# Performance work log

Measured on AMD Instinct MI355X. Metric: run time of the kernel, lower is better.

## Reference

```python
import jax, jax.numpy as jnp
import numpy as np

N = 100_000   # nodes
E = 600_000   # edges per layer (avg degree ~6, ogbn-arxiv-like)
IN, H, C = 128, 256, 40


def _sage_layer(x, src, dst, w_self, w_neigh, b):
    """DGL SAGEConv with mean aggregator: fc_self(x) + fc_neigh(mean_nbr) + b."""
    n = x.shape[0]
    msg = x[src]                                               # [E, d] gather
    agg = jax.ops.segment_sum(msg, dst, num_segments=n)        # [N, d]
    deg = jax.ops.segment_sum(jnp.ones((src.shape[0],), x.dtype), dst,
                              num_segments=n)                  # [N]
    h_neigh = agg / jnp.maximum(deg, 1.0)[:, None]             # mean; 0 if isolated
    return x @ w_self.T + h_neigh @ w_neigh.T + b


def setup_inputs() -> dict:
    key = jax.random.key(0)
    ks = jax.random.split(key, 11)
    s = 0.02
    return {
        "x": jax.random.normal(ks[0], (N, IN), jnp.float32),
        "src1": jax.random.randint(ks[1], (E,), 0, N, jnp.int32),
        "dst1": jax.random.randint(ks[2], (E,), 0, N, jnp.int32),
        "src2": jax.random.randint(ks[3], (E,), 0, N, jnp.int32),
        "dst2": jax.random.randint(ks[4], (E,), 0, N, jnp.int32),
        "w_self1": s * jax.random.normal(ks[5], (H, IN), jnp.float32),
        "w_neigh1": s * jax.random.normal(ks[6], (H, IN), jnp.float32),
        "b1": jnp.zeros((H,), jnp.float32),
        "w_self2": s * jax.random.normal(ks[7], (C, H), jnp.float32),
        "w_neigh2": s * jax.random.normal(ks[8], (C, H), jnp.float32),
        "b2": jnp.zeros((C,), jnp.float32),
    }


def reference(x, src1, dst1, src2, dst2, w_self1, w_neigh1, b1,
              w_self2, w_neigh2, b2):
    h = jax.nn.relu(_sage_layer(x, src1, dst1, w_self1, w_neigh1, b1))
    return _sage_layer(h, src2, dst2, w_self2, w_neigh2, b2)
```

## Files before the change

### kernel.cpp

```cpp
#include <hip/hip_runtime.h>
#include <hip/hip_bf16.h>
#include <cstdint>
#include <cstddef>


#define D_IN 128
#define D_H  256
#define D_C  40

#define NBLK     128
#define NBKT_MAX 392
#define BKT_CAP  2560

typedef __bf16 bf16_t;
typedef __attribute__((ext_vector_type(8))) __bf16 bf16x8;
typedef __attribute__((ext_vector_type(4))) __bf16 bf16x4;
typedef __attribute__((ext_vector_type(4))) float  f32x4;

static constexpr size_t NMAX = 100000;
static constexpr size_t EMAX = 600000;
static constexpr size_t NSC_MAX = (size_t)NBKT_MAX * NBLK;
static constexpr size_t alignup(size_t v) { return (v + 255) & ~size_t(255); }

static constexpr size_t HG1_OFF  = 0;
static constexpr size_t HG2_OFF  = alignup(HG1_OFF + NSC_MAX * 4);
static constexpr size_t BS1_OFF  = alignup(HG2_OFF + NSC_MAX * 4);
static constexpr size_t BS2_OFF  = alignup(BS1_OFF + 512 * 4);
static constexpr size_t RP1_OFF  = alignup(BS2_OFF + 512 * 4);
static constexpr size_t RP2_OFF  = alignup(RP1_OFF + (NMAX + 1) * 4);
static constexpr size_t BKT1_OFF = alignup(RP2_OFF + (NMAX + 1) * 4);
static constexpr size_t BKT2_OFF = alignup(BKT1_OFF + EMAX * 4);
static constexpr size_t XCAT_OFF = alignup(BKT2_OFF + EMAX * 4);
static constexpr size_t P_OFF    = alignup(XCAT_OFF + (NMAX + 64) * 256 * 2);
static constexpr size_t W1F_OFF  = alignup(P_OFF + NMAX * 40 * 2);
static constexpr size_t W2F_OFF  = alignup(W1F_OFF + 32 * 256 * 8 * 2);
static constexpr size_t WS_NEEDED = W2F_OFF + 32 * 80 * 8 * 2;

__global__ __launch_bounds__(256) void k_prep(
    const float* __restrict__ x, bf16_t* __restrict__ xcat,
    const float* __restrict__ ws1, const float* __restrict__ wn1,
    const float* __restrict__ ws2, const float* __restrict__ wn2,
    bf16_t* __restrict__ w1f, bf16_t* __restrict__ w2f,
    const int* __restrict__ dst1, const int* __restrict__ dst2,
    int* __restrict__ hg1, int* __restrict__ hg2,
    int N, int E, int chunk, int nbkt, int nconvx) {
  __shared__ int h[NBKT_MAX];
  int bid = blockIdx.x;

  if (bid < nconvx) {
    int t = bid * 256 + threadIdx.x;
    if (t < N * 16) {
      int row = t >> 4, j = t & 15;
      const float* sp = x + (size_t)row * 128 + j * 8;
      float4 v0 = ((const float4*)sp)[0];
      float4 v1 = ((const float4*)sp)[1];
      bf16x8 o;
      o[0] = (bf16_t)v0.x; o[1] = (bf16_t)v0.y; o[2] = (bf16_t)v0.z; o[3] = (bf16_t)v0.w;
      o[4] = (bf16_t)v1.x; o[5] = (bf16_t)v1.y; o[6] = (bf16_t)v1.z; o[7] = (bf16_t)v1.w;
      *(bf16x8*)(xcat + (size_t)row * 256 + j * 8) = o;
    }
    return;
  }
  bid -= nconvx;

  if (bid < 32) {
    int t = bid * 256 + threadIdx.x;
    {
      int ks4g = t >> 8, col = t & 255;
      int k0 = (ks4g >> 2) * 32 + (ks4g & 3) * 8;
      bf16x8 o;
#pragma unroll
      for (int i = 0; i < 8; ++i) {
        int k = k0 + i;
        float v = (k < 128) ? ws1[col * 128 + k] : wn1[col * 128 + (k - 128)];
        o[i] = (bf16_t)v;
      }
      *(bf16x8*)(w1f + (size_t)t * 8) = o;
    }
    if (t < 32 * 80) {
      int ks4g = t / 80, col = t - ks4g * 80;
      int k0 = (ks4g >> 2) * 32 + (ks4g & 3) * 8;
      bf16x8 o;
#pragma unroll
      for (int i = 0; i < 8; ++i) {
        int k = k0 + i;
        float v = (col < 40) ? ws2[col * 256 + k] : wn2[(col - 40) * 256 + k];
        o[i] = (bf16_t)v;
      }
      *(bf16x8*)(w2f + (size_t)t * 8) = o;
    }
    return;
  }
  bid -= 32;
  {
    const int* dst = (bid >> 7) ? dst2 : dst1;
    int*       hg  = (bid >> 7) ? hg2 : hg1;
    int        cb  = bid & 127;
    for (int i = threadIdx.x; i < nbkt; i += 256) h[i] = 0;
    __syncthreads();
    int beg = cb * chunk, end = min(E, beg + chunk);
    for (int e = beg + threadIdx.x; e < end; e += 256)
      atomicAdd(&h[dst[e] >> 8], 1);
    __syncthreads();
    for (int b = threadIdx.x; b < nbkt; b += 256)
      hg[b * NBLK + cb] = h[b];
  }
}

__global__ void k_scan_block(int* __restrict__ a1, int* __restrict__ a2,
                             int* __restrict__ b1s, int* __restrict__ b2s, int n) {
  int* a    = blockIdx.y ? a2 : a1;
  int* bsum = blockIdx.y ? b2s : b1s;
  __shared__ int lds[256];
  int t = threadIdx.x, i = blockIdx.x * 256 + t;
  int v = (i < n) ? a[i] : 0;
  lds[t] = v;
  __syncthreads();
  for (int off = 1; off < 256; off <<= 1) {
    int add = (t >= off) ? lds[t - off] : 0;
    __syncthreads();
    lds[t] += add;
    __syncthreads();
  }
  if (i < n) a[i] = lds[t] - v;
  if (t == 255) bsum[blockIdx.x] = lds[255];
}

__global__ void k_scat(const int* __restrict__ src1, const int* __restrict__ dst1,
                       const int* __restrict__ src2, const int* __restrict__ dst2,
                       const int* __restrict__ hg1, const int* __restrict__ hg2,
                       const int* __restrict__ b1s, const int* __restrict__ b2s,
                       unsigned* __restrict__ bkt1, unsigned* __restrict__ bkt2,
                       int E, int chunk, int nbkt, int nb) {
  const int* src = blockIdx.y ? src2 : src1;
  const int* dst = blockIdx.y ? dst2 : dst1;
  const int* hg  = blockIdx.y ? hg2 : hg1;
  const int* bs  = blockIdx.y ? b2s : b1s;
  unsigned*  bkt = blockIdx.y ? bkt2 : bkt1;
  const int cb = blockIdx.x, t = threadIdx.x;

  __shared__ int sbuf[256];
  __shared__ int sexcl[256];
  __shared__ int cur[NBKT_MAX];

  int v = (t < nb) ? bs[t] : 0;
  sbuf[t] = v;
  __syncthreads();
  for (int off = 1; off < 256; off <<= 1) {
    int add = (t >= off) ? sbuf[t - off] : 0;
    __syncthreads();
    sbuf[t] += add;
    __syncthreads();
  }
  sexcl[t] = sbuf[t] - v;
  __syncthreads();
  for (int i = t; i < nbkt; i += 256) {
    int idx = i * NBLK + cb;
    cur[i] = hg[idx] + sexcl[idx >> 8];
  }
  __syncthreads();

  int beg = cb * chunk, end = min(E, beg + chunk);
  for (int e = beg + t; e < end; e += 256) {
    int d = dst[e];
    int slot = atomicAdd(&cur[d >> 8], 1);
    bkt[slot] = (unsigned)src[e] | ((unsigned)(d & 255) << 24);
  }
}

__global__ __launch_bounds__(256) void k_bcsr(
    const int* __restrict__ hg1, const int* __restrict__ hg2,
    const int* __restrict__ b1s, const int* __restrict__ b2s,
    const unsigned* bkt1, const unsigned* bkt2,
    int* csr1, int* csr2,
    int* __restrict__ rp1, int* __restrict__ rp2, int E, int N, int nbkt, int nb) {
  const int* hg       = blockIdx.y ? hg2 : hg1;
  const int* bs       = blockIdx.y ? b2s : b1s;
  const unsigned* bkt = blockIdx.y ? bkt2 : bkt1;
  int* csr            = blockIdx.y ? csr2 : csr1;
  int* rowptr         = blockIdx.y ? rp2 : rp1;

  const int b = blockIdx.x, t = threadIdx.x;

  __shared__ int sbuf[256];
  __shared__ int hist[256];
  __shared__ int sc[256];
  __shared__ int cur[256];
  __shared__ int stage[BKT_CAP];
  __shared__ int s_base, s_endp;

  int v0 = (t < nb) ? bs[t] : 0;
  sbuf[t] = v0;
  __syncthreads();
  for (int off_ = 1; off_ < 256; off_ <<= 1) {
    int add = (t >= off_) ? sbuf[t - off_] : 0;
    __syncthreads();
    sbuf[t] += add;
    __syncthreads();
  }
  if (t == 0) {
    int i0 = b * NBLK;
    int e0 = sbuf[i0 >> 8] - ((i0 >> 8) < nb ? bs[i0 >> 8] : 0);
    s_base = hg[i0] + e0;
    if (b == nbkt - 1) {
      s_endp = E;
    } else {
      int i1 = (b + 1) * NBLK;
      int e1 = sbuf[i1 >> 8] - ((i1 >> 8) < nb ? bs[i1 >> 8] : 0);
      s_endp = hg[i1] + e1;
    }
  }
  hist[t] = 0;
  __syncthreads();
  const int base = s_base, endp = s_endp;
  const int cnt  = endp - base;

  for (int i = t; i < cnt; i += 256)
    atomicAdd(&hist[bkt[base + i] >> 24], 1);
  __syncthreads();

  int v = hist[t];
  sc[t] = v;
  __syncthreads();
  for (int off_ = 1; off_ < 256; off_ <<= 1) {
    int add = (t >= off_) ? sc[t - off_] : 0;
    __syncthreads();
    sc[t] += add;
    __syncthreads();
  }
  int excl = sc[t] - v;

  int node = b * 256 + t;
  if (node < N) rowptr[node] = base + excl;
  if (b == nbkt - 1 && t == 0) rowptr[N] = E;
  cur[t] = excl;
  __syncthreads();

  for (int i = t; i < cnt; i += 256) {
    unsigned u = bkt[base + i];
    int slot = atomicAdd(&cur[u >> 24], 1);
    if (slot < BKT_CAP) stage[slot] = (int)(u & 0xFFFFFFu);
  }
  __syncthreads();
  for (int i = t; i < cnt; i += 256)
    csr[base + i] = stage[i];
}

__global__ void k_agg1(bf16_t* __restrict__ xcat, const int* __restrict__ rowptr,
                       const int* __restrict__ csr, int N) {
  int t = blockIdx.x * 256 + threadIdx.x;
  int node = t >> 4, l = t & 15;
  if (node >= N) return;
  int beg = rowptr[node], end = rowptr[node + 1];
  float acc[8] = {0.f, 0.f, 0.f, 0.f, 0.f, 0.f, 0.f, 0.f};
  for (int e = beg; e < end; e += 4) {
    int e1 = e + 1 < end ? e + 1 : e;
    int e2 = e + 2 < end ? e + 2 : e;
    int e3 = e + 3 < end ? e + 3 : e;
    float m1 = e + 1 < end ? 1.f : 0.f;
    float m2 = e + 2 < end ? 1.f : 0.f;
    float m3 = e + 3 < end ? 1.f : 0.f;
    int s0 = csr[e], s1 = csr[e1], s2 = csr[e2], s3 = csr[e3];
    bf16x8 v0 = *(const bf16x8*)(xcat + (size_t)s0 * 256 + l * 8);
    bf16x8 v1 = *(const bf16x8*)(xcat + (size_t)s1 * 256 + l * 8);
    bf16x8 v2 = *(const bf16x8*)(xcat + (size_t)s2 * 256 + l * 8);
    bf16x8 v3 = *(const bf16x8*)(xcat + (size_t)s3 * 256 + l * 8);
#pragma unroll
    for (int i = 0; i < 8; ++i)
      acc[i] += (float)v0[i] + m1 * (float)v1[i] + m2 * (float)v2[i] + m3 * (float)v3[i];
  }
  float rd = (end > beg) ? 1.0f / (float)(end - beg) : 0.0f;
  bf16x8 o;
#pragma unroll
  for (int i = 0; i < 8; ++i) o[i] = (bf16_t)(acc[i] * rd);
  *(bf16x8*)(xcat + (size_t)node * 256 + 128 + l * 8) = o;
}

__global__ __launch_bounds__(256, 3) void k_fused(
    const bf16_t* __restrict__ xcat, const bf16_t* __restrict__ w1f,
    const float* __restrict__ b1, const bf16_t* __restrict__ w2f,
    const float* __restrict__ b2v, float* __restrict__ out,
    bf16_t* __restrict__ p, int N) {
  __shared__ __align__(16) char lds[32768];
  const int tid  = (int)threadIdx.x;
  const int wv   = tid >> 6;
  const int lane = tid & 63;
  const int lr   = lane & 15;
  const int lg   = lane >> 4;
  const int c0   = wv * 64;
  const int m0   = (int)blockIdx.x * 64;

  {
    const char* tb = (const char*)(xcat + (size_t)m0 * 256);
#pragma unroll
    for (int i = 0; i < 8; ++i) {
      int L   = i * 4096 + tid * 16;
      int row = L >> 9;
      int c   = L & 511;
      int so  = (row << 9) | (c ^ ((row & 7) << 4));
      __builtin_amdgcn_global_load_lds(
          (const __attribute__((address_space(1))) void*)(tb + so),
          (__attribute__((address_space(3))) void*)(lds + L), 16, 0, 0);
    }
  }

  bf16x8 wfc[4];
#pragma unroll
  for (int wb = 0; wb < 4; ++wb)
    wfc[wb] = *(const bf16x8*)(w1f + ((size_t)(0 * 4 + lg) * 256 +
                                      (c0 + wb * 16 + lr)) * 8);
  __syncthreads();

  bf16x8 axc[4];
#pragma unroll
  for (int rb = 0; rb < 4; ++rb) {
    int lrow = rb * 16 + lr;
    axc[rb] = *(const bf16x8*)(lds + lrow * 512 +
                               ((0 * 64 + lg * 16) ^ ((lrow & 7) << 4)));
  }

  f32x4 acc[4][4] = {};
#pragma unroll
  for (int ks = 0; ks < 8; ++ks) {
    bf16x8 wfn[4], axn[4];
    if (ks < 7) {
#pragma unroll
      for (int wb = 0; wb < 4; ++wb)
        wfn[wb] = *(const bf16x8*)(w1f + ((size_t)((ks + 1) * 4 + lg) * 256 +
                                          (c0 + wb * 16 + lr)) * 8);
#pragma unroll
      for (int rb = 0; rb < 4; ++rb) {
        int lrow = rb * 16 + lr;
        axn[rb] = *(const bf16x8*)(lds + lrow * 512 +
                                   (((ks + 1) * 64 + lg * 16) ^ ((lrow & 7) << 4)));
      }
    }
#pragma unroll
    for (int wb = 0; wb < 4; ++wb)
#pragma unroll
      for (int rb = 0; rb < 4; ++rb)
        acc[wb][rb] = __builtin_amdgcn_mfma_f32_16x16x32_bf16(
            wfc[wb], axc[rb], acc[wb][rb], 0, 0, 0);
    if (ks < 7) {
#pragma unroll
      for (int i = 0; i < 4; ++i) { wfc[i] = wfn[i]; axc[i] = axn[i]; }
    }
  }

  __syncthreads();

#pragma unroll
  for (int wb = 0; wb < 4; ++wb) {
    float4 b4 = *(const float4*)(b1 + c0 + wb * 16 + lg * 4);
#pragma unroll
    for (int rb = 0; rb < 4; ++rb) {
      int xrow = rb * 16 + lr;
      bf16x4 o;
      o[0] = (bf16_t)fmaxf(acc[wb][rb][0] + b4.x, 0.f);
      o[1] = (bf16_t)fmaxf(acc[wb][rb][1] + b4.y, 0.f);
      o[2] = (bf16_t)fmaxf(acc[wb][rb][2] + b4.z, 0.f);
      o[3] = (bf16_t)fmaxf(acc[wb][rb][3] + b4.w, 0.f);
      *(bf16x4*)(lds + xrow * 512 +
                 ((c0 * 2 + wb * 32 + lg * 8) ^ ((xrow & 7) << 4))) = o;
    }
  }
  __syncthreads();

  const int arow = wv * 16 + lr;
  bf16x8 hfc = *(const bf16x8*)(lds + arow * 512 +
                                ((0 * 64 + lg * 16) ^ ((arow & 7) << 4)));
  bf16x8 w2c[5];
#pragma unroll
  for (int wb = 0; wb < 5; ++wb)
    w2c[wb] = *(const bf16x8*)(w2f + ((size_t)(0 * 4 + lg) * 80 +
                                      (wb * 16 + lr)) * 8);

  f32x4 acc2[5] = {};
#pragma unroll
  for (int ks = 0; ks < 8; ++ks) {
    bf16x8 hfn, w2n[5];
    if (ks < 7) {
      hfn = *(const bf16x8*)(lds + arow * 512 +
                             (((ks + 1) * 64 + lg * 16) ^ ((arow & 7) << 4)));
#pragma unroll
      for (int wb = 0; wb < 5; ++wb)
        w2n[wb] = *(const bf16x8*)(w2f + ((size_t)((ks + 1) * 4 + lg) * 80 +
                                          (wb * 16 + lr)) * 8);
    }
#pragma unroll
    for (int wb = 0; wb < 5; ++wb)
      acc2[wb] = __builtin_amdgcn_mfma_f32_16x16x32_bf16(
          w2c[wb], hfc, acc2[wb], 0, 0, 0);
    if (ks < 7) {
      hfc = hfn;
#pragma unroll
      for (int i = 0; i < 5; ++i) w2c[i] = w2n[i];
    }
  }

  const int r = m0 + wv * 16 + lr;
  if (r < N) {
#pragma unroll
    for (int wb = 0; wb < 5; ++wb) {
      int col0 = wb * 16 + lg * 4;
      f32x4 v = acc2[wb];
      if (col0 < 40) {
        float4 b4 = *(const float4*)(b2v + col0);
        v[0] += b4.x; v[1] += b4.y; v[2] += b4.z; v[3] += b4.w;
        *(f32x4*)(out + (size_t)r * 40 + col0) = v;
      } else {
        bf16x4 o;
        o[0] = (bf16_t)v[0]; o[1] = (bf16_t)v[1];
        o[2] = (bf16_t)v[2]; o[3] = (bf16_t)v[3];
        *(bf16x4*)(p + (size_t)r * 40 + (col0 - 40)) = o;
      }
    }
  }
}

__global__ void k_agg2fin(const bf16_t* __restrict__ p, const int* __restrict__ rowptr,
                          const int* __restrict__ csr, float* __restrict__ out, int N) {
  int t = blockIdx.x * 256 + threadIdx.x;
  int node = t / 10, l = t - node * 10;
  if (node >= N) return;
  int beg = rowptr[node], end = rowptr[node + 1];
  float a0 = 0.f, a1 = 0.f, a2 = 0.f, a3 = 0.f;
  for (int e = beg; e < end; e += 4) {
    int e1 = e + 1 < end ? e + 1 : e;
    int e2 = e + 2 < end ? e + 2 : e;
    int e3 = e + 3 < end ? e + 3 : e;
    float m1 = e + 1 < end ? 1.f : 0.f;
    float m2 = e + 2 < end ? 1.f : 0.f;
    float m3 = e + 3 < end ? 1.f : 0.f;
    int s0 = csr[e], s1 = csr[e1], s2 = csr[e2], s3 = csr[e3];
    bf16x4 v0 = *(const bf16x4*)(p + (size_t)s0 * 40 + l * 4);
    bf16x4 v1 = *(const bf16x4*)(p + (size_t)s1 * 40 + l * 4);
    bf16x4 v2 = *(const bf16x4*)(p + (size_t)s2 * 40 + l * 4);
    bf16x4 v3 = *(const bf16x4*)(p + (size_t)s3 * 40 + l * 4);
    a0 += (float)v0[0] + m1 * (float)v1[0] + m2 * (float)v2[0] + m3 * (float)v3[0];
    a1 += (float)v0[1] + m1 * (float)v1[1] + m2 * (float)v2[1] + m3 * (float)v3[1];
    a2 += (float)v0[2] + m1 * (float)v1[2] + m2 * (float)v2[2] + m3 * (float)v3[2];
    a3 += (float)v0[3] + m1 * (float)v1[3] + m2 * (float)v2[3] + m3 * (float)v3[3];
  }
  float rd = (end > beg) ? 1.0f / (float)(end - beg) : 0.0f;
  float* o = out + (size_t)node * 40 + l * 4;
  float4 cur = *(const float4*)o;
  cur.x += a0 * rd;
  cur.y += a1 * rd;
  cur.z += a2 * rd;
  cur.w += a3 * rd;
  *(float4*)o = cur;
}

extern "C" void kernel_launch(void* const* d_in, const int* in_sizes, int n_in,
                              void* d_out, int out_size, void* d_ws, size_t ws_size,
                              hipStream_t stream) {
  const float* x    = (const float*)d_in[0];
  const int*   src1 = (const int*)d_in[1];
  const int*   dst1 = (const int*)d_in[2];
  const int*   src2 = (const int*)d_in[3];
  const int*   dst2 = (const int*)d_in[4];
  const float* ws1  = (const float*)d_in[5];
  const float* wn1  = (const float*)d_in[6];
  const float* b1   = (const float*)d_in[7];
  const float* ws2  = (const float*)d_in[8];
  const float* wn2  = (const float*)d_in[9];
  const float* b2   = (const float*)d_in[10];
  float*       out  = (float*)d_out;

  const int N = in_sizes[0] / D_IN;
  const int E = in_sizes[1];
  if (ws_size < WS_NEEDED) return;

  char*     ws   = (char*)d_ws;
  int*      hg1  = (int*)(ws + HG1_OFF);
  int*      hg2  = (int*)(ws + HG2_OFF);
  int*      bs1  = (int*)(ws + BS1_OFF);
  int*      bs2  = (int*)(ws + BS2_OFF);
  int*      rp1  = (int*)(ws + RP1_OFF);
  int*      rp2  = (int*)(ws + RP2_OFF);
  unsigned* bkt1 = (unsigned*)(ws + BKT1_OFF);
  unsigned* bkt2 = (unsigned*)(ws + BKT2_OFF);
  int*      csr1 = (int*)(ws + BKT1_OFF);
  int*      csr2 = (int*)(ws + BKT2_OFF);
  bf16_t*   xcat = (bf16_t*)(ws + XCAT_OFF);
  bf16_t*   p    = (bf16_t*)(ws + P_OFF);
  bf16_t*   w1f  = (bf16_t*)(ws + W1F_OFF);
  bf16_t*   w2f  = (bf16_t*)(ws + W2F_OFF);

  const int nbkt  = (N + 255) >> 8;
  const int chunk = (E + NBLK - 1) / NBLK;
  const int nsc   = nbkt * NBLK;
  const int nscb  = (nsc + 255) / 256;
  const int nconvx = (N * 16 + 255) / 256;
  const int ntiles = (N + 63) / 64;

  k_prep<<<nconvx + 32 + 2 * NBLK, 256, 0, stream>>>(
      x, xcat, ws1, wn1, ws2, wn2, w1f, w2f, dst1, dst2, hg1, hg2,
      N, E, chunk, nbkt, nconvx);

  k_scan_block<<<dim3(nscb, 2), 256, 0, stream>>>(hg1, hg2, bs1, bs2, nsc);
  k_scat<<<dim3(NBLK, 2), 256, 0, stream>>>(src1, dst1, src2, dst2, hg1, hg2,
                                            bs1, bs2, bkt1, bkt2, E, chunk, nbkt, nscb);
  k_bcsr<<<dim3(nbkt, 2), 256, 0, stream>>>(hg1, hg2, bs1, bs2, bkt1, bkt2,
                                            csr1, csr2, rp1, rp2, E, N, nbkt, nscb);

  k_agg1<<<(N * 16 + 255) / 256, 256, 0, stream>>>(xcat, rp1, csr1, N);
  k_fused<<<ntiles, 256, 0, stream>>>(xcat, w1f, b1, w2f, b2, out, p, N);
  k_agg2fin<<<(N * 10 + 255) / 256, 256, 0, stream>>>(p, rp2, csr2, out, N);
}
```

Baseline: 133.2 us.

## Fuse layer-1 neighbor aggregation into bucket CSR build kernel

The layer-1 mean aggregation now runs inside k_bcsr for the layer-1 blocks. Each block reads source indices straight from its LDS staging buffer and per-node degrees from the shared histogram, instead of writing csr1 and rowptr1 to global memory and launching a separate k_agg1. This removes one kernel launch and the global round trip of the layer-1 CSR. In exchange, the layer-1 half of the grid holds about 391 blocks that each loop over 256 nodes, 16 at a time, so aggregation parallelism is coarser and the layer-2 and layer-1 blocks become unbalanced.

Measured after the change: 135.5 us. Within noise of the previous version (+1.8%).

```diff
diff --git a/kernel.cpp b/kernel.cpp
--- a/kernel.cpp
+++ b/kernel.cpp
@@ -26,8 +26,7 @@
 static constexpr size_t HG2_OFF  = alignup(HG1_OFF + NSC_MAX * 4);
 static constexpr size_t BS1_OFF  = alignup(HG2_OFF + NSC_MAX * 4);
 static constexpr size_t BS2_OFF  = alignup(BS1_OFF + 512 * 4);
-static constexpr size_t RP1_OFF  = alignup(BS2_OFF + 512 * 4);
-static constexpr size_t RP2_OFF  = alignup(RP1_OFF + (NMAX + 1) * 4);
+static constexpr size_t RP2_OFF  = alignup(BS2_OFF + 512 * 4);
 static constexpr size_t BKT1_OFF = alignup(RP2_OFF + (NMAX + 1) * 4);
 static constexpr size_t BKT2_OFF = alignup(BKT1_OFF + EMAX * 4);
 static constexpr size_t XCAT_OFF = alignup(BKT2_OFF + EMAX * 4);
@@ -172,13 +171,12 @@
     const int* __restrict__ hg1, const int* __restrict__ hg2,
     const int* __restrict__ b1s, const int* __restrict__ b2s,
     const unsigned* bkt1, const unsigned* bkt2,
-    int* csr1, int* csr2,
-    int* __restrict__ rp1, int* __restrict__ rp2, int E, int N, int nbkt, int nb) {
+    int* csr2, int* __restrict__ rp2,
+    bf16_t* __restrict__ xcat,
+    int E, int N, int nbkt, int nb) {
   const int* hg       = blockIdx.y ? hg2 : hg1;
   const int* bs       = blockIdx.y ? b2s : b1s;
   const unsigned* bkt = blockIdx.y ? bkt2 : bkt1;
-  int* csr            = blockIdx.y ? csr2 : csr1;
-  int* rowptr         = blockIdx.y ? rp2 : rp1;
 
   const int b = blockIdx.x, t = threadIdx.x;
 
@@ -229,10 +227,6 @@
     __syncthreads();
   }
   int excl = sc[t] - v;
-
-  int node = b * 256 + t;
-  if (node < N) rowptr[node] = base + excl;
-  if (b == nbkt - 1 && t == 0) rowptr[N] = E;
   cur[t] = excl;
   __syncthreads();
 
@@ -242,38 +236,47 @@
     if (slot < BKT_CAP) stage[slot] = (int)(u & 0xFFFFFFu);
   }
   __syncthreads();
-  for (int i = t; i < cnt; i += 256)
-    csr[base + i] = stage[i];
-}
-
-__global__ void k_agg1(bf16_t* __restrict__ xcat, const int* __restrict__ rowptr,
-                       const int* __restrict__ csr, int N) {
-  int t = blockIdx.x * 256 + threadIdx.x;
-  int node = t >> 4, l = t & 15;
-  if (node >= N) return;
-  int beg = rowptr[node], end = rowptr[node + 1];
-  float acc[8] = {0.f, 0.f, 0.f, 0.f, 0.f, 0.f, 0.f, 0.f};
-  for (int e = beg; e < end; e += 4) {
-    int e1 = e + 1 < end ? e + 1 : e;
-    int e2 = e + 2 < end ? e + 2 : e;
-    int e3 = e + 3 < end ? e + 3 : e;
-    float m1 = e + 1 < end ? 1.f : 0.f;
-    float m2 = e + 2 < end ? 1.f : 0.f;
-    float m3 = e + 3 < end ? 1.f : 0.f;
-    int s0 = csr[e], s1 = csr[e1], s2 = csr[e2], s3 = csr[e3];
-    bf16x8 v0 = *(const bf16x8*)(xcat + (size_t)s0 * 256 + l * 8);
-    bf16x8 v1 = *(const bf16x8*)(xcat + (size_t)s1 * 256 + l * 8);
-    bf16x8 v2 = *(const bf16x8*)(xcat + (size_t)s2 * 256 + l * 8);
-    bf16x8 v3 = *(const bf16x8*)(xcat + (size_t)s3 * 256 + l * 8);
-#pragma unroll
-    for (int i = 0; i < 8; ++i)
-      acc[i] += (float)v0[i] + m1 * (float)v1[i] + m2 * (float)v2[i] + m3 * (float)v3[i];
-  }
-  float rd = (end > beg) ? 1.0f / (float)(end - beg) : 0.0f;
-  bf16x8 o;
-#pragma unroll
-  for (int i = 0; i < 8; ++i) o[i] = (bf16_t)(acc[i] * rd);
-  *(bf16x8*)(xcat + (size_t)node * 256 + 128 + l * 8) = o;
+
+  if (blockIdx.y) {
+    int node = b * 256 + t;
+    if (node < N) rp2[node] = base + excl;
+    if (b == nbkt - 1 && t == 0) rp2[N] = E;
+    for (int i = t; i < cnt; i += 256)
+      csr2[base + i] = stage[i];
+    return;
+  }
+
+  const int l = t & 15;
+  for (int g = 0; g < 16; ++g) {
+    int nl   = g * 16 + (t >> 4);
+    int node = b * 256 + nl;
+    if (node >= N) continue;
+    int deg = hist[nl];
+    int beg = sc[nl] - deg;
+    float acc[8] = {0.f, 0.f, 0.f, 0.f, 0.f, 0.f, 0.f, 0.f};
+    for (int e = 0; e < deg; e += 4) {
+      int e1 = e + 1 < deg ? e + 1 : e;
+      int e2 = e + 2 < deg ? e + 2 : e;
+      int e3 = e + 3 < deg ? e + 3 : e;
+      float m1 = e + 1 < deg ? 1.f : 0.f;
+      float m2 = e + 2 < deg ? 1.f : 0.f;
+      float m3 = e + 3 < deg ? 1.f : 0.f;
+      int s0 = stage[beg + e], s1 = stage[beg + e1];
+      int s2 = stage[beg + e2], s3 = stage[beg + e3];
+      bf16x8 v0_ = *(const bf16x8*)(xcat + (size_t)s0 * 256 + l * 8);
+      bf16x8 v1_ = *(const bf16x8*)(xcat + (size_t)s1 * 256 + l * 8);
+      bf16x8 v2_ = *(const bf16x8*)(xcat + (size_t)s2 * 256 + l * 8);
+      bf16x8 v3_ = *(const bf16x8*)(xcat + (size_t)s3 * 256 + l * 8);
+#pragma unroll
+      for (int i = 0; i < 8; ++i)
+        acc[i] += (float)v0_[i] + m1 * (float)v1_[i] + m2 * (float)v2_[i] + m3 * (float)v3_[i];
+    }
+    float rd = deg > 0 ? 1.0f / (float)deg : 0.0f;
+    bf16x8 o;
+#pragma unroll
+    for (int i = 0; i < 8; ++i) o[i] = (bf16_t)(acc[i] * rd);
+    *(bf16x8*)(xcat + (size_t)node * 256 + 128 + l * 8) = o;
+  }
 }
 
 __global__ __launch_bounds__(256, 3) void k_fused(
@@ -477,11 +480,9 @@
   int*      hg2  = (int*)(ws + HG2_OFF);
   int*      bs1  = (int*)(ws + BS1_OFF);
   int*      bs2  = (int*)(ws + BS2_OFF);
-  int*      rp1  = (int*)(ws + RP1_OFF);
   int*      rp2  = (int*)(ws + RP2_OFF);
   unsigned* bkt1 = (unsigned*)(ws + BKT1_OFF);
   unsigned* bkt2 = (unsigned*)(ws + BKT2_OFF);
-  int*      csr1 = (int*)(ws + BKT1_OFF);
   int*      csr2 = (int*)(ws + BKT2_OFF);
   bf16_t*   xcat = (bf16_t*)(ws + XCAT_OFF);
   bf16_t*   p    = (bf16_t*)(ws + P_OFF);
@@ -503,9 +504,8 @@
   k_scat<<<dim3(NBLK, 2), 256, 0, stream>>>(src1, dst1, src2, dst2, hg1, hg2,
                                             bs1, bs2, bkt1, bkt2, E, chunk, nbkt, nscb);
   k_bcsr<<<dim3(nbkt, 2), 256, 0, stream>>>(hg1, hg2, bs1, bs2, bkt1, bkt2,
-                                            csr1, csr2, rp1, rp2, E, N, nbkt, nscb);
-
-  k_agg1<<<(N * 16 + 255) / 256, 256, 0, stream>>>(xcat, rp1, csr1, N);
+                                            csr2, rp2, xcat, E, N, nbkt, nscb);
+
   k_fused<<<ntiles, 256, 0, stream>>>(xcat, w1f, b1, w2f, b2, out, p, N);
   k_agg2fin<<<(N * 10 + 255) / 256, 256, 0, stream>>>(p, rp2, csr2, out, N);
 }
```
